# Kernel optimization log

Measured on AMD Instinct MI355X. Metric: run time of the kernel, lower is better.

The kernel has to match this reference:

```python
import jax, jax.numpy as jnp
import numpy as np

B, DIM, H, W = 8, 96, 256, 256
NH, WS, SS = 3, 8, 4
HD = DIM // NH
SCALE = HD ** -0.5
N = WS * WS  # tokens per window


def _rel_pos_log(ws):
    # [N, N, 2] signed log relative coordinates (matches get_relative_positions)
    coords = np.stack(np.meshgrid(np.arange(ws), np.arange(ws), indexing='ij'))
    cf = coords.reshape(2, -1)
    rel = (cf[:, :, None] - cf[:, None, :]).transpose(1, 2, 0).astype(np.float32)
    return np.sign(rel) * np.log1p(np.abs(rel))


def _attn_mask(Hh, Ww, ws, ss):
    # Swin shifted-window mask: [nW, N, N] with 0 / -100
    img = np.zeros((Hh, Ww))
    cnt = 0
    sl = (slice(0, -ws), slice(-ws, -ss), slice(-ss, None))
    for h in sl:
        for w in sl:
            img[h, w] = cnt
            cnt += 1
    mw = img.reshape(Hh // ws, ws, Ww // ws, ws).transpose(0, 2, 1, 3).reshape(-1, ws * ws)
    am = mw[:, None, :] - mw[:, :, None]
    return np.where(am != 0, -100.0, 0.0).astype(np.float32)


REL_POS = jnp.asarray(_rel_pos_log(WS))        # [N, N, 2]
ATTN_MASK = jnp.asarray(_attn_mask(H, W, WS, SS))  # [nW, N, N]


def setup_inputs() -> dict:
    key = jax.random.key(0)
    ks = jax.random.split(key, 8)
    s = 0.02
    return {
        'x': jax.random.normal(ks[0], (B, DIM, H, W), jnp.float32),
        'V_w': jax.random.normal(ks[1], (DIM, DIM), jnp.float32) * s,
        'V_b': jnp.zeros((DIM,), jnp.float32),
        'QK_w': jax.random.normal(ks[2], (2 * DIM, DIM), jnp.float32) * s,
        'QK_b': jnp.zeros((2 * DIM,), jnp.float32),
        'proj_w': jax.random.normal(ks[3], (DIM, DIM), jnp.float32) * s,
        'proj_b': jnp.zeros((DIM,), jnp.float32),
        'dw_w': jax.random.normal(ks[4], (DIM, 5, 5), jnp.float32) * s,
        'dw_b': jnp.zeros((DIM,), jnp.float32),
        'meta_w1': jax.random.normal(ks[5], (256, 2), jnp.float32) * 0.1,
        'meta_b1': jnp.zeros((256,), jnp.float32),
        'meta_w2': jax.random.normal(ks[6], (NH, 256), jnp.float32) * 0.1,
        'meta_b2': jnp.zeros((NH,), jnp.float32),
    }


def reference(x, V_w, V_b, QK_w, QK_b, proj_w, proj_b, dw_w, dw_b,
              meta_w1, meta_b1, meta_w2, meta_b2):
    # 1x1 convs as channel matmuls
    V = jnp.einsum('bchw,oc->bohw', x, V_w) + V_b[None, :, None, None]
    QK = jnp.einsum('bchw,oc->bohw', x, QK_w) + QK_b[None, :, None, None]
    qkv = jnp.concatenate([QK, V], axis=1).transpose(0, 2, 3, 1)  # [B,H,W,3C]
    # cyclic shift
    qkv = jnp.roll(qkv, (-SS, -SS), axis=(1, 2))
    # window partition -> [B*nW, N, 3C]
    xw = qkv.reshape(B, H // WS, WS, W // WS, WS, 3 * DIM)
    xw = xw.transpose(0, 1, 3, 2, 4, 5).reshape(-1, N, 3 * DIM)
    qkv3 = xw.reshape(-1, N, 3, NH, HD).transpose(2, 0, 3, 1, 4)  # [3, B_, nh, N, hd]
    q, k, v = qkv3[0] * SCALE, qkv3[1], qkv3[2]
    attn = jnp.einsum('whnd,whmd->whnm', q, k)  # [B_, nh, N, N]
    # MLP relative-position bias
    bias = jax.nn.relu(REL_POS @ meta_w1.T + meta_b1) @ meta_w2.T + meta_b2  # [N,N,nh]
    attn = attn + bias.transpose(2, 0, 1)[None]
    nW = ATTN_MASK.shape[0]
    attn = attn.reshape(B, nW, NH, N, N) + ATTN_MASK[None, :, None]
    attn = jax.nn.softmax(attn, axis=-1).reshape(-1, NH, N, N)
    xo = jnp.einsum('whnm,whmd->wnhd', attn, v).reshape(-1, N, DIM)
    # window reverse -> [B,H,W,C]
    xr = xo.reshape(B, H // WS, W // WS, WS, WS, DIM)
    xr = xr.transpose(0, 1, 3, 2, 4, 5).reshape(B, H, W, DIM)
    xr = jnp.roll(xr, (SS, SS), axis=(1, 2)).transpose(0, 3, 1, 2)  # [B,C,H,W]
    # depthwise 5x5 conv with reflect padding on V
    Vp = jnp.pad(V, ((0, 0), (0, 0), (2, 2), (2, 2)), mode='reflect')
    conv_out = jax.lax.conv_general_dilated(
        Vp, dw_w.reshape(DIM, 1, 5, 5), (1, 1), 'VALID',
        feature_group_count=DIM,
        dimension_numbers=('NCHW', 'OIHW', 'NCHW')) + dw_b[None, :, None, None]
    out = jnp.einsum('bchw,oc->bohw', conv_out + xr, proj_w) + proj_b[None, :, None, None]
    return out
```

## Files before the change

### kernel.cpp

```cpp
#include <hip/hip_runtime.h>
#include <hip/hip_bf16.h>

#define HW 65536
#define SCALE_Q 0.17677669529663687f

typedef __bf16 bf16x8 __attribute__((ext_vector_type(8)));
typedef float f32x4 __attribute__((ext_vector_type(4)));

__global__ void bias_kernel(const float* __restrict__ w1, const float* __restrict__ b1,
                            const float* __restrict__ w2, const float* __restrict__ b2,
                            float* __restrict__ biasF) {
    int gid = blockIdx.x * blockDim.x + threadIdx.x;
    if (gid >= 12288) return;
    int lane = gid & 63, r = (gid >> 6) & 3, ni = (gid >> 8) & 3, mi = (gid >> 10) & 3, h = gid >> 12;
    int i = mi * 16 + ((lane >> 4) << 2) + r;
    int j = ni * 16 + (lane & 15);
    float di = (float)((i >> 3) - (j >> 3));
    float dj = (float)((i & 7) - (j & 7));
    float r0 = (di > 0.f ? 1.f : (di < 0.f ? -1.f : 0.f)) * log1pf(fabsf(di));
    float r1 = (dj > 0.f ? 1.f : (dj < 0.f ? -1.f : 0.f)) * log1pf(fabsf(dj));
    float acc = 0.f;
    for (int t = 0; t < 256; ++t) {
        float u = fmaf(w1[2 * t], r0, fmaf(w1[2 * t + 1], r1, b1[t]));
        u = fmaxf(u, 0.f);
        acc = fmaf(w2[h * 256 + t], u, acc);
    }
    biasF[gid] = acc + b2[h];
}

__global__ void wtrans_kernel(const float* __restrict__ QK_w, const float* __restrict__ V_w,
                              const float* __restrict__ proj_w,
                              __bf16* __restrict__ Whi, __bf16* __restrict__ Wlo,
                              __bf16* __restrict__ WpHi, __bf16* __restrict__ WpLo) {
    int idx = blockIdx.x * blockDim.x + threadIdx.x;
    if (idx < 288 * 96) {
        int oo = idx / 96, c = idx - oo * 96;
        int h = oo / 96, rem = oo - h * 96, grp = rem >> 5, d = rem & 31;
        float w = (grp == 0) ? QK_w[(h * 32 + d) * 96 + c]
                : (grp == 1) ? QK_w[(96 + h * 32 + d) * 96 + c]
                             : V_w[(h * 32 + d) * 96 + c];
        __bf16 hi = (__bf16)w;
        Whi[idx] = hi;
        Wlo[idx] = (__bf16)(w - (float)hi);
    } else if (idx < 288 * 96 + 96 * 96) {
        int rdx = idx - 288 * 96;
        float w = proj_w[rdx];
        __bf16 hi = (__bf16)w;
        WpHi[rdx] = hi;
        WpLo[rdx] = (__bf16)(w - (float)hi);
    }
}

template <bool XRB>
__global__ __launch_bounds__(256, 4) void fused_qkv_attn(
    const float* __restrict__ x,
    const __bf16* __restrict__ Whi, const __bf16* __restrict__ Wlo,
    const float* __restrict__ QK_b, const float* __restrict__ V_b,
    const float* __restrict__ biasF,
    unsigned short* __restrict__ Vout, void* __restrict__ xrv) {
    __shared__ __align__(16) char lds[39936];
    int tid = threadIdx.x;
    int w4 = tid >> 6;
    int lane = tid & 63;
    int l16 = lane & 15;
    int g8 = (lane >> 4) << 3;
    int g4 = (lane >> 4) << 2;
    int bx0 = blockIdx.x;
    int bxs = (bx0 & 7) * 256 + (bx0 >> 3);
    int b = bxs >> 8;
    int wh = (bxs >> 3) & 31;
    int ww0 = (bxs & 7) << 2;
    int wh8 = wh << 3;
    int ww = ww0 + w4;
    int ti = lane >> 3, tj = lane & 7;
    int ph = (wh8 + ti + 4) & 255;
    int pw = ((ww << 3) + tj + 4) & 255;
    int pos   = ph * 256 + pw;
    int pos_s = (wh8 + ti) * 256 + (ww << 3) + tj;

    const float* xb = x + (size_t)b * 96 * HW;
    bf16x8 Ah[4][3];
#pragma unroll
    for (int mi = 0; mi < 4; ++mi) {
        int t = mi * 16 + l16;
        int py = (wh8 + (t >> 3) + 4) & 255;
        int px = ((ww << 3) + (t & 7) + 4) & 255;
        const float* xp = xb + py * 256 + px + (size_t)g8 * HW;
#pragma unroll
        for (int ks = 0; ks < 3; ++ks)
#pragma unroll
            for (int e = 0; e < 8; ++e)
                Ah[mi][ks][e] = (__bf16)xp[(size_t)(ks * 32 + e) * HW];
    }

    char* hb = lds + w4 * 9984;
    __bf16* slab = (__bf16*)hb;
    __bf16* Vt   = (__bf16*)(hb + 5120);
    float*  Xr   = (float*)hb;

    bool bhh = (wh == 31), bww = (ww == 31);
    int rc[4];
#pragma unroll
    for (int ni = 0; ni < 4; ++ni) {
        int t = ni * 16 + l16;
        rc[ni] = (bhh ? (((t >> 3) < 4) ? 1 : 2) : 0) * 3 + (bww ? (((t & 7) < 4) ? 1 : 2) : 0);
    }

#pragma unroll 1
    for (int h = 0; h < 3; ++h) {
        bf16x8 Qf[4], Kf[4];
        {
            f32x4 acc[4][2];
#pragma unroll
            for (int mi = 0; mi < 4; ++mi)
#pragma unroll
                for (int ni = 0; ni < 2; ++ni) acc[mi][ni] = (f32x4){0.f, 0.f, 0.f, 0.f};
            __builtin_amdgcn_s_setprio(1);
#pragma unroll
            for (int ks = 0; ks < 3; ++ks)
#pragma unroll
                for (int ni = 0; ni < 2; ++ni) {
                    bf16x8 Bh = *(const bf16x8*)(Whi + (h * 96 + ni * 16 + l16) * 96 + ks * 32 + g8);
#pragma unroll
                    for (int mi = 0; mi < 4; ++mi)
                        acc[mi][ni] = __builtin_amdgcn_mfma_f32_16x16x32_bf16(Ah[mi][ks], Bh, acc[mi][ni], 0, 0, 0);
                }
            __builtin_amdgcn_s_setprio(0);
#pragma unroll
            for (int ni = 0; ni < 2; ++ni) {
                float bias = QK_b[h * 32 + ni * 16 + l16];
#pragma unroll
                for (int mi = 0; mi < 4; ++mi)
#pragma unroll
                    for (int r = 0; r < 4; ++r)
                        slab[(mi * 16 + g4 + r) * 40 + ni * 16 + l16] = (__bf16)((acc[mi][ni][r] + bias) * SCALE_Q);
            }
#pragma unroll
            for (int mi = 0; mi < 4; ++mi) Qf[mi] = *(const bf16x8*)(slab + (mi * 16 + l16) * 40 + g8);
        }
        {
            f32x4 acc[4][2];
#pragma unroll
            for (int mi = 0; mi < 4; ++mi)
#pragma unroll
                for (int ni = 0; ni < 2; ++ni) acc[mi][ni] = (f32x4){0.f, 0.f, 0.f, 0.f};
            __builtin_amdgcn_s_setprio(1);
#pragma unroll
            for (int ks = 0; ks < 3; ++ks)
#pragma unroll
                for (int ni = 0; ni < 2; ++ni) {
                    bf16x8 Bh = *(const bf16x8*)(Whi + (h * 96 + 32 + ni * 16 + l16) * 96 + ks * 32 + g8);
#pragma unroll
                    for (int mi = 0; mi < 4; ++mi)
                        acc[mi][ni] = __builtin_amdgcn_mfma_f32_16x16x32_bf16(Ah[mi][ks], Bh, acc[mi][ni], 0, 0, 0);
                }
            __builtin_amdgcn_s_setprio(0);
#pragma unroll
            for (int ni = 0; ni < 2; ++ni) {
                float bias = QK_b[96 + h * 32 + ni * 16 + l16];
#pragma unroll
                for (int mi = 0; mi < 4; ++mi)
#pragma unroll
                    for (int r = 0; r < 4; ++r)
                        slab[(mi * 16 + g4 + r) * 40 + ni * 16 + l16] = (__bf16)(acc[mi][ni][r] + bias);
            }
#pragma unroll
            for (int mi = 0; mi < 4; ++mi) Kf[mi] = *(const bf16x8*)(slab + (mi * 16 + l16) * 40 + g8);
        }
        {
            f32x4 acc[4][2];
#pragma unroll
            for (int mi = 0; mi < 4; ++mi)
#pragma unroll
                for (int ni = 0; ni < 2; ++ni) acc[mi][ni] = (f32x4){0.f, 0.f, 0.f, 0.f};
            __builtin_amdgcn_s_setprio(1);
#pragma unroll
            for (int ks = 0; ks < 3; ++ks)
#pragma unroll
                for (int ni = 0; ni < 2; ++ni) {
                    bf16x8 Bh = *(const bf16x8*)(Whi + (h * 96 + 64 + ni * 16 + l16) * 96 + ks * 32 + g8);
#pragma unroll
                    for (int mi = 0; mi < 4; ++mi)
                        acc[mi][ni] = __builtin_amdgcn_mfma_f32_16x16x32_bf16(Ah[mi][ks], Bh, acc[mi][ni], 0, 0, 0);
                }
            __builtin_amdgcn_s_setprio(0);
#pragma unroll
            for (int ni = 0; ni < 2; ++ni) {
                float bias = V_b[h * 32 + ni * 16 + l16];
#pragma unroll
                for (int mi = 0; mi < 4; ++mi)
#pragma unroll
                    for (int r = 0; r < 4; ++r)
                        Vt[(ni * 16 + l16) * 72 + mi * 16 + g4 + r] = (__bf16)(acc[mi][ni][r] + bias);
            }
        }
#pragma unroll
        for (int d = 0; d < 32; ++d)
            Vout[(size_t)(b * 96 + h * 32 + d) * HW + pos_s] = ((const unsigned short*)Vt)[d * 72 + lane];

        f32x4 sc[4][4];
        __builtin_amdgcn_s_setprio(1);
#pragma unroll
        for (int mi = 0; mi < 4; ++mi)
#pragma unroll
            for (int ni = 0; ni < 4; ++ni) {
                sc[mi][ni] = (f32x4){0.f, 0.f, 0.f, 0.f};
                sc[mi][ni] = __builtin_amdgcn_mfma_f32_16x16x32_bf16(Qf[mi], Kf[ni], sc[mi][ni], 0, 0, 0);
            }
        __builtin_amdgcn_s_setprio(0);
        const float* bF = biasF + h * 4096;
#pragma unroll
        for (int mi = 0; mi < 4; ++mi)
#pragma unroll
            for (int r = 0; r < 4; ++r) {
                int row = mi * 16 + g4 + r;
                float s0 = sc[mi][0][r] + bF[((mi * 4 + 0) * 4 + r) * 64 + lane];
                float s1 = sc[mi][1][r] + bF[((mi * 4 + 1) * 4 + r) * 64 + lane];
                float s2 = sc[mi][2][r] + bF[((mi * 4 + 2) * 4 + r) * 64 + lane];
                float s3 = sc[mi][3][r] + bF[((mi * 4 + 3) * 4 + r) * 64 + lane];
                if (bhh || bww) {
                    int rr = (bhh ? (((row >> 3) < 4) ? 1 : 2) : 0) * 3 +
                             (bww ? (((row & 7) < 4) ? 1 : 2) : 0);
                    if (rr != rc[0]) s0 -= 100.f;
                    if (rr != rc[1]) s1 -= 100.f;
                    if (rr != rc[2]) s2 -= 100.f;
                    if (rr != rc[3]) s3 -= 100.f;
                }
                float mm = fmaxf(fmaxf(s0, s1), fmaxf(s2, s3));
                mm = fmaxf(mm, __shfl_xor(mm, 1));
                mm = fmaxf(mm, __shfl_xor(mm, 2));
                mm = fmaxf(mm, __shfl_xor(mm, 4));
                mm = fmaxf(mm, __shfl_xor(mm, 8));
                float e0 = __expf(s0 - mm), e1 = __expf(s1 - mm);
                float e2 = __expf(s2 - mm), e3 = __expf(s3 - mm);
                float sum = e0 + e1 + e2 + e3;
                sum += __shfl_xor(sum, 1);
                sum += __shfl_xor(sum, 2);
                sum += __shfl_xor(sum, 4);
                sum += __shfl_xor(sum, 8);
                float inv = 1.f / sum;
                sc[mi][0][r] = e0 * inv;
                sc[mi][1][r] = e1 * inv;
                sc[mi][2][r] = e2 * inv;
                sc[mi][3][r] = e3 * inv;
            }
        f32x4 po[4][2];
#pragma unroll
        for (int mi = 0; mi < 4; ++mi)
#pragma unroll
            for (int ni = 0; ni < 2; ++ni) po[mi][ni] = (f32x4){0.f, 0.f, 0.f, 0.f};
#pragma unroll
        for (int ks = 0; ks < 2; ++ks) {
#pragma unroll
            for (int mi = 0; mi < 4; ++mi)
#pragma unroll
                for (int r = 0; r < 4; ++r) {
                    int row = mi * 16 + g4 + r;
                    slab[row * 40 + l16]      = (__bf16)sc[mi][ks * 2 + 0][r];
                    slab[row * 40 + 16 + l16] = (__bf16)sc[mi][ks * 2 + 1][r];
                }
            bf16x8 Vf[2], Pf;
#pragma unroll
            for (int ni = 0; ni < 2; ++ni)
                Vf[ni] = *(const bf16x8*)(Vt + (ni * 16 + l16) * 72 + ks * 32 + g8);
            __builtin_amdgcn_s_setprio(1);
#pragma unroll
            for (int mi = 0; mi < 4; ++mi) {
                Pf = *(const bf16x8*)(slab + (mi * 16 + l16) * 40 + g8);
#pragma unroll
                for (int ni = 0; ni < 2; ++ni)
                    po[mi][ni] = __builtin_amdgcn_mfma_f32_16x16x32_bf16(Pf, Vf[ni], po[mi][ni], 0, 0, 0);
            }
            __builtin_amdgcn_s_setprio(0);
        }
#pragma unroll
        for (int mi = 0; mi < 4; ++mi)
#pragma unroll
            for (int ni = 0; ni < 2; ++ni)
#pragma unroll
                for (int r = 0; r < 4; ++r)
                    Xr[(mi * 16 + g4 + r) * 36 + ni * 16 + l16] = po[mi][ni][r];
        if constexpr (XRB) {
            unsigned short* xrg = (unsigned short*)xrv + (size_t)(b * 96 + h * 32) * HW + pos;
#pragma unroll
            for (int c4 = 0; c4 < 8; ++c4) {
                f32x4 v = *(const f32x4*)(Xr + lane * 36 + c4 * 4);
#pragma unroll
                for (int j = 0; j < 4; ++j) {
                    __bf16 t = (__bf16)v[j];
                    xrg[(size_t)(c4 * 4 + j) * HW] = *(unsigned short*)&t;
                }
            }
        } else {
            float* xrg = (float*)xrv + (size_t)(b * 96 + h * 32) * HW + pos;
#pragma unroll
            for (int c4 = 0; c4 < 8; ++c4) {
                f32x4 v = *(const f32x4*)(Xr + lane * 36 + c4 * 4);
                xrg[(size_t)(c4 * 4 + 0) * HW] = v[0];
                xrg[(size_t)(c4 * 4 + 1) * HW] = v[1];
                xrg[(size_t)(c4 * 4 + 2) * HW] = v[2];
                xrg[(size_t)(c4 * 4 + 3) * HW] = v[3];
            }
        }
    }
}

template <bool XRB>
__global__ __launch_bounds__(256) void dwproj_kernel(
    const __hip_bfloat16* __restrict__ Vs, const float* __restrict__ dw_w,
    const float* __restrict__ dw_b, const __bf16* __restrict__ WpHi,
    const __bf16* __restrict__ WpLo, const float* __restrict__ pb,
    const void* __restrict__ xrv, float* __restrict__ T) {
    __shared__ __align__(16) __bf16 Ts[13312];
    int bx0 = blockIdx.x;
    int bx = (bx0 & 7) * 512 + (bx0 >> 3);
    int half = bx & 1, h = (bx >> 1) & 255, b = bx >> 9;
    int w0 = half << 7;
    int tid = threadIdx.x;
    for (int task = tid; task < 1536; task += 256) {
        int c = task >> 4, g = task & 15;
        int wbase = w0 + (g << 3);
        const __hip_bfloat16* Vp = Vs + (size_t)(b * 96 + c) * HW;
        const float* wt = dw_w + c * 25;
        float acc[8];
        float bias = dw_b[c];
#pragma unroll
        for (int i = 0; i < 8; ++i) acc[i] = bias;
        bool fast = (wbase >= 8) && (wbase <= 240);
#pragma unroll
        for (int dy = -2; dy <= 2; ++dy) {
            int hh = h + dy;
            hh = hh < 0 ? -hh : (hh > 255 ? 510 - hh : hh);
            int hs = (hh + 252) & 255;
            const __hip_bfloat16* row = Vp + hs * 256;
            float xv[12];
            if (fast) {
                const uint* rp = (const uint*)(row + (wbase - 6));
#pragma unroll
                for (int g2 = 0; g2 < 6; ++g2) {
                    uint u = rp[g2];
                    xv[2 * g2]     = __uint_as_float(u << 16);
                    xv[2 * g2 + 1] = __uint_as_float(u & 0xffff0000u);
                }
            } else {
#pragma unroll
                for (int idx = 0; idx < 12; ++idx) {
                    int cw = wbase - 2 + idx;
                    cw = cw < 0 ? -cw : (cw > 255 ? 510 - cw : cw);
                    int cs = (cw + 252) & 255;
                    uint u = *(const unsigned short*)(row + cs);
                    xv[idx] = __uint_as_float(u << 16);
                }
            }
            const float* w5 = wt + (dy + 2) * 5;
#pragma unroll
            for (int dx = 0; dx < 5; ++dx) {
                float wv = w5[dx];
#pragma unroll
                for (int i = 0; i < 8; ++i) acc[i] = fmaf(wv, xv[i + dx], acc[i]);
            }
        }
        if constexpr (XRB) {
            const unsigned short* xp = (const unsigned short*)xrv + (size_t)(b * 96 + c) * HW + h * 256 + wbase;
            uint4 u = *(const uint4*)xp;
            acc[0] += __uint_as_float(u.x << 16);
            acc[1] += __uint_as_float(u.x & 0xffff0000u);
            acc[2] += __uint_as_float(u.y << 16);
            acc[3] += __uint_as_float(u.y & 0xffff0000u);
            acc[4] += __uint_as_float(u.z << 16);
            acc[5] += __uint_as_float(u.z & 0xffff0000u);
            acc[6] += __uint_as_float(u.w << 16);
            acc[7] += __uint_as_float(u.w & 0xffff0000u);
        } else {
            const float* xp = (const float*)xrv + (size_t)(b * 96 + c) * HW + h * 256;
            f32x4 x0 = *(const f32x4*)(xp + wbase);
            f32x4 x1 = *(const f32x4*)(xp + wbase + 4);
#pragma unroll
            for (int i = 0; i < 4; ++i) { acc[i] += x0[i]; acc[4 + i] += x1[i]; }
        }
#pragma unroll
        for (int i = 0; i < 8; ++i) Ts[(g * 8 + i) * 104 + c] = (__bf16)acc[i];
    }
    __syncthreads();
    int lane = tid & 63;
    int l16 = lane & 15;
    int g8 = (lane >> 4) << 3;
    int g4 = (lane >> 4) << 2;
    int wv = tid >> 6;
    f32x4 po[2][6];
#pragma unroll
    for (int mi = 0; mi < 2; ++mi)
#pragma unroll
        for (int ni = 0; ni < 6; ++ni) po[mi][ni] = (f32x4){0.f, 0.f, 0.f, 0.f};
#pragma unroll
    for (int ks = 0; ks < 3; ++ks) {
        bf16x8 Av[2];
#pragma unroll
        for (int mi = 0; mi < 2; ++mi)
            Av[mi] = *(const bf16x8*)(Ts + (wv * 32 + mi * 16 + l16) * 104 + ks * 32 + g8);
#pragma unroll
        for (int ni = 0; ni < 6; ++ni) {
            int o = ni * 16 + l16;
            bf16x8 Bh = *(const bf16x8*)(WpHi + o * 96 + ks * 32 + g8);
            bf16x8 Bl = *(const bf16x8*)(WpLo + o * 96 + ks * 32 + g8);
#pragma unroll
            for (int mi = 0; mi < 2; ++mi) {
                po[mi][ni] = __builtin_amdgcn_mfma_f32_16x16x32_bf16(Av[mi], Bh, po[mi][ni], 0, 0, 0);
                po[mi][ni] = __builtin_amdgcn_mfma_f32_16x16x32_bf16(Av[mi], Bl, po[mi][ni], 0, 0, 0);
            }
        }
    }
#pragma unroll
    for (int ni = 0; ni < 6; ++ni) {
        int o = ni * 16 + l16;
        float bias = pb[o];
#pragma unroll
        for (int mi = 0; mi < 2; ++mi) {
            f32x4 v = po[mi][ni];
            v[0] += bias; v[1] += bias; v[2] += bias; v[3] += bias;
            *(f32x4*)(T + (size_t)(b * 96 + o) * HW + h * 256 + w0 + wv * 32 + mi * 16 + g4) = v;
        }
    }
}

extern "C" void kernel_launch(void* const* d_in, const int* in_sizes, int n_in,
                              void* d_out, int out_size, void* d_ws, size_t ws_size,
                              hipStream_t stream) {
    const float* x      = (const float*)d_in[0];
    const float* V_w    = (const float*)d_in[1];
    const float* V_b    = (const float*)d_in[2];
    const float* QK_w   = (const float*)d_in[3];
    const float* QK_b   = (const float*)d_in[4];
    const float* proj_w = (const float*)d_in[5];
    const float* proj_b = (const float*)d_in[6];
    const float* dw_w   = (const float*)d_in[7];
    const float* dw_b   = (const float*)d_in[8];
    const float* mw1    = (const float*)d_in[9];
    const float* mb1    = (const float*)d_in[10];
    const float* mw2    = (const float*)d_in[11];
    const float* mb2    = (const float*)d_in[12];
    float* out = (float*)d_out;

    char* ws = (char*)d_ws;
    const size_t VB = 100663296;
    bool xrb = (ws_size >= 2 * VB + 49152 + 2 * 55296 + 2 * 18432);

    __hip_bfloat16* Vbuf = (__hip_bfloat16*)ws;
    size_t off = VB;
    unsigned short* xr16 = nullptr;
    if (xrb) { xr16 = (unsigned short*)(ws + off); off += VB; }
    float*  biasF = (float*)(ws + off); off += 49152;
    __bf16* Whi   = (__bf16*)(ws + off); off += 55296;
    __bf16* Wlo   = (__bf16*)(ws + off); off += 55296;
    __bf16* WpHi  = (__bf16*)(ws + off); off += 18432;
    __bf16* WpLo  = (__bf16*)(ws + off);

    bias_kernel<<<48, 256, 0, stream>>>(mw1, mb1, mw2, mb2, biasF);
    wtrans_kernel<<<144, 256, 0, stream>>>(QK_w, V_w, proj_w, Whi, Wlo, WpHi, WpLo);
    if (xrb) {
        fused_qkv_attn<true><<<2048, 256, 0, stream>>>(x, Whi, Wlo, QK_b, V_b, biasF,
                                                       (unsigned short*)Vbuf, (void*)xr16);
        dwproj_kernel<true><<<4096, 256, 0, stream>>>(Vbuf, dw_w, dw_b, WpHi, WpLo, proj_b,
                                                      (const void*)xr16, out);
    } else {
        fused_qkv_attn<false><<<2048, 256, 0, stream>>>(x, Whi, Wlo, QK_b, V_b, biasF,
                                                        (unsigned short*)Vbuf, (void*)out);
        dwproj_kernel<false><<<4096, 256, 0, stream>>>(Vbuf, dw_w, dw_b, WpHi, WpLo, proj_b,
                                                       (const void*)out, out);
    }
}
```

Baseline: 676.0 us.

## Pre-transpose x into window-major bf16 layout and store attention output window-major

Adds an xprep kernel that gathers the shifted-window tiles of x into a contiguous bf16 window-major buffer, so the fused attention kernel loads its A fragments with vector loads instead of strided scalar fp32 gathers. The attention output is also written in a window-major bf16 layout through LDS, and the depthwise/projection kernel reads that layout back. The projection kernel moves to 512 threads with one 16-row tile per wave. This costs an extra kernel launch, an extra full pass over x, and a third 100MB workspace buffer, and the new path only runs when the workspace is large enough.

Result: slower. 729.1 us (+7.8%).

```diff
diff --git a/kernel.cpp b/kernel.cpp
--- a/kernel.cpp
+++ b/kernel.cpp
@@ -51,9 +51,37 @@
     }
 }
 
-template <bool XRB>
+__global__ __launch_bounds__(256) void xprep_kernel(const float* __restrict__ x,
+                                                    __bf16* __restrict__ xT) {
+    __shared__ __bf16 Xs[26624];
+    int tid = threadIdx.x;
+    int bxs = blockIdx.x;
+    int b = bxs >> 8;
+    int wh = (bxs >> 3) & 31;
+    int ww0 = (bxs & 7) << 2;
+    int wh8 = wh << 3, wb8 = ww0 << 3;
+    const float* xb = x + (size_t)b * 96 * HW;
+    for (int idx = tid; idx < 24576; idx += 256) {
+        int c = idx >> 8, r = (idx >> 5) & 7, col = idx & 31;
+        int pph = (wh8 + r + 4) & 255;
+        int ppw = (wb8 + col + 4) & 255;
+        Xs[(col >> 3) * 6656 + (r * 8 + (col & 7)) * 104 + c] =
+            (__bf16)xb[(size_t)c * HW + pph * 256 + ppw];
+    }
+    __syncthreads();
+    int win = tid >> 6, t = tid & 63;
+    const __bf16* row = Xs + win * 6656 + t * 104;
+    __bf16* dst = xT + (size_t)(b * 1024 + wh * 32 + ww0 + win) * 6144 + t * 8;
+#pragma unroll
+    for (int ks = 0; ks < 3; ++ks)
+#pragma unroll
+        for (int g = 0; g < 4; ++g)
+            *(bf16x8*)(dst + (ks * 4 + g) * 512) = *(const bf16x8*)(row + ks * 32 + g * 8);
+}
+
+template <int MODE>
 __global__ __launch_bounds__(256, 4) void fused_qkv_attn(
-    const float* __restrict__ x,
+    const float* __restrict__ x, const __bf16* __restrict__ xT,
     const __bf16* __restrict__ Whi, const __bf16* __restrict__ Wlo,
     const float* __restrict__ QK_b, const float* __restrict__ V_b,
     const float* __restrict__ biasF,
@@ -72,25 +100,35 @@
     int ww0 = (bxs & 7) << 2;
     int wh8 = wh << 3;
     int ww = ww0 + w4;
+    int wl = wh * 32 + ww;
     int ti = lane >> 3, tj = lane & 7;
     int ph = (wh8 + ti + 4) & 255;
     int pw = ((ww << 3) + tj + 4) & 255;
     int pos   = ph * 256 + pw;
     int pos_s = (wh8 + ti) * 256 + (ww << 3) + tj;
 
-    const float* xb = x + (size_t)b * 96 * HW;
     bf16x8 Ah[4][3];
-#pragma unroll
-    for (int mi = 0; mi < 4; ++mi) {
-        int t = mi * 16 + l16;
-        int py = (wh8 + (t >> 3) + 4) & 255;
-        int px = ((ww << 3) + (t & 7) + 4) & 255;
-        const float* xp = xb + py * 256 + px + (size_t)g8 * HW;
-#pragma unroll
-        for (int ks = 0; ks < 3; ++ks)
-#pragma unroll
-            for (int e = 0; e < 8; ++e)
-                Ah[mi][ks][e] = (__bf16)xp[(size_t)(ks * 32 + e) * HW];
+    if constexpr (MODE == 2) {
+        const __bf16* xTw = xT + (size_t)(b * 1024 + wl) * 6144;
+#pragma unroll
+        for (int mi = 0; mi < 4; ++mi)
+#pragma unroll
+            for (int ks = 0; ks < 3; ++ks)
+                Ah[mi][ks] = *(const bf16x8*)(xTw + (ks * 4 + (lane >> 4)) * 512 + (mi * 16 + l16) * 8);
+    } else {
+        const float* xb = x + (size_t)b * 96 * HW;
+#pragma unroll
+        for (int mi = 0; mi < 4; ++mi) {
+            int t = mi * 16 + l16;
+            int py = (wh8 + (t >> 3) + 4) & 255;
+            int px = ((ww << 3) + (t & 7) + 4) & 255;
+            const float* xp = xb + py * 256 + px + (size_t)g8 * HW;
+#pragma unroll
+            for (int ks = 0; ks < 3; ++ks)
+#pragma unroll
+                for (int e = 0; e < 8; ++e)
+                    Ah[mi][ks][e] = (__bf16)xp[(size_t)(ks * 32 + e) * HW];
+        }
     }
 
     char* hb = lds + w4 * 9984;
@@ -273,40 +311,58 @@
             }
             __builtin_amdgcn_s_setprio(0);
         }
-#pragma unroll
-        for (int mi = 0; mi < 4; ++mi)
-#pragma unroll
-            for (int ni = 0; ni < 2; ++ni)
-#pragma unroll
-                for (int r = 0; r < 4; ++r)
-                    Xr[(mi * 16 + g4 + r) * 36 + ni * 16 + l16] = po[mi][ni][r];
-        if constexpr (XRB) {
-            unsigned short* xrg = (unsigned short*)xrv + (size_t)(b * 96 + h * 32) * HW + pos;
-#pragma unroll
-            for (int c4 = 0; c4 < 8; ++c4) {
-                f32x4 v = *(const f32x4*)(Xr + lane * 36 + c4 * 4);
-#pragma unroll
-                for (int j = 0; j < 4; ++j) {
-                    __bf16 t = (__bf16)v[j];
-                    xrg[(size_t)(c4 * 4 + j) * HW] = *(unsigned short*)&t;
-                }
-            }
+        if constexpr (MODE == 2) {
+            __bf16* Xrt = slab;
+#pragma unroll
+            for (int mi = 0; mi < 4; ++mi)
+#pragma unroll
+                for (int ni = 0; ni < 2; ++ni)
+#pragma unroll
+                    for (int r = 0; r < 4; ++r)
+                        Xrt[(ni * 16 + l16) * 72 + mi * 16 + g4 + r] = (__bf16)po[mi][ni][r];
+            int d = lane >> 1, half = lane & 1;
+            const unsigned short* src = (const unsigned short*)Xrt + d * 72 + half * 32;
+            unsigned short* dst = (unsigned short*)xrv +
+                ((size_t)(b * 96 + h * 32 + d) * 1024 + wl) * 64 + half * 32;
+#pragma unroll
+            for (int i = 0; i < 4; ++i)
+                *(uint4*)(dst + i * 8) = *(const uint4*)(src + i * 8);
         } else {
-            float* xrg = (float*)xrv + (size_t)(b * 96 + h * 32) * HW + pos;
-#pragma unroll
-            for (int c4 = 0; c4 < 8; ++c4) {
-                f32x4 v = *(const f32x4*)(Xr + lane * 36 + c4 * 4);
-                xrg[(size_t)(c4 * 4 + 0) * HW] = v[0];
-                xrg[(size_t)(c4 * 4 + 1) * HW] = v[1];
-                xrg[(size_t)(c4 * 4 + 2) * HW] = v[2];
-                xrg[(size_t)(c4 * 4 + 3) * HW] = v[3];
+#pragma unroll
+            for (int mi = 0; mi < 4; ++mi)
+#pragma unroll
+                for (int ni = 0; ni < 2; ++ni)
+#pragma unroll
+                    for (int r = 0; r < 4; ++r)
+                        Xr[(mi * 16 + g4 + r) * 36 + ni * 16 + l16] = po[mi][ni][r];
+            if constexpr (MODE == 1) {
+                unsigned short* xrg = (unsigned short*)xrv + (size_t)(b * 96 + h * 32) * HW + pos;
+#pragma unroll
+                for (int c4 = 0; c4 < 8; ++c4) {
+                    f32x4 v = *(const f32x4*)(Xr + lane * 36 + c4 * 4);
+#pragma unroll
+                    for (int j = 0; j < 4; ++j) {
+                        __bf16 t = (__bf16)v[j];
+                        xrg[(size_t)(c4 * 4 + j) * HW] = *(unsigned short*)&t;
+                    }
+                }
+            } else {
+                float* xrg = (float*)xrv + (size_t)(b * 96 + h * 32) * HW + pos;
+#pragma unroll
+                for (int c4 = 0; c4 < 8; ++c4) {
+                    f32x4 v = *(const f32x4*)(Xr + lane * 36 + c4 * 4);
+                    xrg[(size_t)(c4 * 4 + 0) * HW] = v[0];
+                    xrg[(size_t)(c4 * 4 + 1) * HW] = v[1];
+                    xrg[(size_t)(c4 * 4 + 2) * HW] = v[2];
+                    xrg[(size_t)(c4 * 4 + 3) * HW] = v[3];
+                }
             }
         }
     }
 }
 
-template <bool XRB>
-__global__ __launch_bounds__(256) void dwproj_kernel(
+template <int MODE>
+__global__ __launch_bounds__(512) void dwproj_kernel(
     const __hip_bfloat16* __restrict__ Vs, const float* __restrict__ dw_w,
     const float* __restrict__ dw_b, const __bf16* __restrict__ WpHi,
     const __bf16* __restrict__ WpLo, const float* __restrict__ pb,
@@ -317,7 +373,7 @@
     int half = bx & 1, h = (bx >> 1) & 255, b = bx >> 9;
     int w0 = half << 7;
     int tid = threadIdx.x;
-    for (int task = tid; task < 1536; task += 256) {
+    for (int task = tid; task < 1536; task += 512) {
         int c = task >> 4, g = task & 15;
         int wbase = w0 + (g << 3);
         const __hip_bfloat16* Vp = Vs + (size_t)(b * 96 + c) * HW;
@@ -360,7 +416,23 @@
                 for (int i = 0; i < 8; ++i) acc[i] = fmaf(wv, xv[i + dx], acc[i]);
             }
         }
-        if constexpr (XRB) {
+        if constexpr (MODE == 2) {
+            int hs2 = (h + 252) & 255;
+            int ps2 = (wbase + 252) & 255;
+            int wrow = (hs2 >> 3) * 32;
+            int rowoff = (hs2 & 7) * 8;
+            const unsigned short* base = (const unsigned short*)xrv + (size_t)(b * 96 + c) * HW;
+            uint2 A = *(const uint2*)(base + (size_t)(wrow + (ps2 >> 3)) * 64 + rowoff + 4);
+            uint2 B = *(const uint2*)(base + (size_t)(wrow + (wbase >> 3)) * 64 + rowoff);
+            acc[0] += __uint_as_float(A.x << 16);
+            acc[1] += __uint_as_float(A.x & 0xffff0000u);
+            acc[2] += __uint_as_float(A.y << 16);
+            acc[3] += __uint_as_float(A.y & 0xffff0000u);
+            acc[4] += __uint_as_float(B.x << 16);
+            acc[5] += __uint_as_float(B.x & 0xffff0000u);
+            acc[6] += __uint_as_float(B.y << 16);
+            acc[7] += __uint_as_float(B.y & 0xffff0000u);
+        } else if constexpr (MODE == 1) {
             const unsigned short* xp = (const unsigned short*)xrv + (size_t)(b * 96 + c) * HW + h * 256 + wbase;
             uint4 u = *(const uint4*)xp;
             acc[0] += __uint_as_float(u.x << 16);
@@ -387,39 +459,28 @@
     int g8 = (lane >> 4) << 3;
     int g4 = (lane >> 4) << 2;
     int wv = tid >> 6;
-    f32x4 po[2][6];
-#pragma unroll
-    for (int mi = 0; mi < 2; ++mi)
-#pragma unroll
-        for (int ni = 0; ni < 6; ++ni) po[mi][ni] = (f32x4){0.f, 0.f, 0.f, 0.f};
+    f32x4 po[6];
+#pragma unroll
+    for (int ni = 0; ni < 6; ++ni) po[ni] = (f32x4){0.f, 0.f, 0.f, 0.f};
 #pragma unroll
     for (int ks = 0; ks < 3; ++ks) {
-        bf16x8 Av[2];
-#pragma unroll
-        for (int mi = 0; mi < 2; ++mi)
-            Av[mi] = *(const bf16x8*)(Ts + (wv * 32 + mi * 16 + l16) * 104 + ks * 32 + g8);
+        bf16x8 Av = *(const bf16x8*)(Ts + (wv * 16 + l16) * 104 + ks * 32 + g8);
 #pragma unroll
         for (int ni = 0; ni < 6; ++ni) {
             int o = ni * 16 + l16;
             bf16x8 Bh = *(const bf16x8*)(WpHi + o * 96 + ks * 32 + g8);
             bf16x8 Bl = *(const bf16x8*)(WpLo + o * 96 + ks * 32 + g8);
-#pragma unroll
-            for (int mi = 0; mi < 2; ++mi) {
-                po[mi][ni] = __builtin_amdgcn_mfma_f32_16x16x32_bf16(Av[mi], Bh, po[mi][ni], 0, 0, 0);
-                po[mi][ni] = __builtin_amdgcn_mfma_f32_16x16x32_bf16(Av[mi], Bl, po[mi][ni], 0, 0, 0);
-            }
+            po[ni] = __builtin_amdgcn_mfma_f32_16x16x32_bf16(Av, Bh, po[ni], 0, 0, 0);
+            po[ni] = __builtin_amdgcn_mfma_f32_16x16x32_bf16(Av, Bl, po[ni], 0, 0, 0);
         }
     }
 #pragma unroll
     for (int ni = 0; ni < 6; ++ni) {
         int o = ni * 16 + l16;
         float bias = pb[o];
-#pragma unroll
-        for (int mi = 0; mi < 2; ++mi) {
-            f32x4 v = po[mi][ni];
-            v[0] += bias; v[1] += bias; v[2] += bias; v[3] += bias;
-            *(f32x4*)(T + (size_t)(b * 96 + o) * HW + h * 256 + w0 + wv * 32 + mi * 16 + g4) = v;
-        }
+        f32x4 v = po[ni];
+        v[0] += bias; v[1] += bias; v[2] += bias; v[3] += bias;
+        *(f32x4*)(T + (size_t)(b * 96 + o) * HW + h * 256 + w0 + wv * 16 + g4) = v;
     }
 }
 
@@ -443,12 +504,15 @@
 
     char* ws = (char*)d_ws;
     const size_t VB = 100663296;
-    bool xrb = (ws_size >= 2 * VB + 49152 + 2 * 55296 + 2 * 18432);
+    const size_t TAB = 49152 + 2 * 55296 + 2 * 18432;
+    int mode = (ws_size >= 3 * VB + TAB) ? 2 : (ws_size >= 2 * VB + TAB) ? 1 : 0;
 
     __hip_bfloat16* Vbuf = (__hip_bfloat16*)ws;
     size_t off = VB;
     unsigned short* xr16 = nullptr;
-    if (xrb) { xr16 = (unsigned short*)(ws + off); off += VB; }
+    __bf16* xT = nullptr;
+    if (mode >= 1) { xr16 = (unsigned short*)(ws + off); off += VB; }
+    if (mode == 2) { xT = (__bf16*)(ws + off); off += VB; }
     float*  biasF = (float*)(ws + off); off += 49152;
     __bf16* Whi   = (__bf16*)(ws + off); off += 55296;
     __bf16* Wlo   = (__bf16*)(ws + off); off += 55296;
@@ -457,15 +521,21 @@
 
     bias_kernel<<<48, 256, 0, stream>>>(mw1, mb1, mw2, mb2, biasF);
     wtrans_kernel<<<144, 256, 0, stream>>>(QK_w, V_w, proj_w, Whi, Wlo, WpHi, WpLo);
-    if (xrb) {
-        fused_qkv_attn<true><<<2048, 256, 0, stream>>>(x, Whi, Wlo, QK_b, V_b, biasF,
-                                                       (unsigned short*)Vbuf, (void*)xr16);
-        dwproj_kernel<true><<<4096, 256, 0, stream>>>(Vbuf, dw_w, dw_b, WpHi, WpLo, proj_b,
-                                                      (const void*)xr16, out);
+    if (mode == 2) {
+        xprep_kernel<<<2048, 256, 0, stream>>>(x, xT);
+        fused_qkv_attn<2><<<2048, 256, 0, stream>>>(x, xT, Whi, Wlo, QK_b, V_b, biasF,
+                                                    (unsigned short*)Vbuf, (void*)xr16);
+        dwproj_kernel<2><<<4096, 512, 0, stream>>>(Vbuf, dw_w, dw_b, WpHi, WpLo, proj_b,
+                                                   (const void*)xr16, out);
+    } else if (mode == 1) {
+        fused_qkv_attn<1><<<2048, 256, 0, stream>>>(x, nullptr, Whi, Wlo, QK_b, V_b, biasF,
+                                                    (unsigned short*)Vbuf, (void*)xr16);
+        dwproj_kernel<1><<<4096, 512, 0, stream>>>(Vbuf, dw_w, dw_b, WpHi, WpLo, proj_b,
+                                                   (const void*)xr16, out);
     } else {
-        fused_qkv_attn<false><<<2048, 256, 0, stream>>>(x, Whi, Wlo, QK_b, V_b, biasF,
-                                                        (unsigned short*)Vbuf, (void*)out);
-        dwproj_kernel<false><<<4096, 256, 0, stream>>>(Vbuf, dw_w, dw_b, WpHi, WpLo, proj_b,
-                                                       (const void*)out, out);
+        fused_qkv_attn<0><<<2048, 256, 0, stream>>>(x, nullptr, Whi, Wlo, QK_b, V_b, biasF,
+                                                    (unsigned short*)Vbuf, (void*)out);
+        dwproj_kernel<0><<<4096, 512, 0, stream>>>(Vbuf, dw_w, dw_b, WpHi, WpLo, proj_b,
+                                                   (const void*)out, out);
     }
 }
```

## Store attention output in window-major bf16 layout and swizzle dwproj LDS tile

Applied to the files above, without the earlier changes.

The attention kernel now transposes its bf16 window output through LDS and writes each channel's 64-token window as contiguous 16-byte vector stores in a window-major layout. The old path was scattered 2-byte stores strided by HW per channel. The dwproj kernel reads this layout back, splitting each 8-pixel chunk across two shifted windows. Its LDS staging tile also gets an XOR swizzle to cut bank conflicts on the strided writes and MFMA operand reads. The cost is more complex address arithmetic and narrower 8-byte gathered loads in dwproj.

New measurement: 646.6 us (median of 2 runs). 4.4% less time.

```diff
diff --git a/kernel.cpp b/kernel.cpp
--- a/kernel.cpp
+++ b/kernel.cpp
@@ -51,7 +51,7 @@
     }
 }
 
-template <bool XRB>
+template <int MODE>
 __global__ __launch_bounds__(256, 4) void fused_qkv_attn(
     const float* __restrict__ x,
     const __bf16* __restrict__ Whi, const __bf16* __restrict__ Wlo,
@@ -72,6 +72,7 @@
     int ww0 = (bxs & 7) << 2;
     int wh8 = wh << 3;
     int ww = ww0 + w4;
+    int wl = wh * 32 + ww;
     int ti = lane >> 3, tj = lane & 7;
     int ph = (wh8 + ti + 4) & 255;
     int pw = ((ww << 3) + tj + 4) & 255;
@@ -273,25 +274,30 @@
             }
             __builtin_amdgcn_s_setprio(0);
         }
-#pragma unroll
-        for (int mi = 0; mi < 4; ++mi)
-#pragma unroll
-            for (int ni = 0; ni < 2; ++ni)
-#pragma unroll
-                for (int r = 0; r < 4; ++r)
-                    Xr[(mi * 16 + g4 + r) * 36 + ni * 16 + l16] = po[mi][ni][r];
-        if constexpr (XRB) {
-            unsigned short* xrg = (unsigned short*)xrv + (size_t)(b * 96 + h * 32) * HW + pos;
-#pragma unroll
-            for (int c4 = 0; c4 < 8; ++c4) {
-                f32x4 v = *(const f32x4*)(Xr + lane * 36 + c4 * 4);
-#pragma unroll
-                for (int j = 0; j < 4; ++j) {
-                    __bf16 t = (__bf16)v[j];
-                    xrg[(size_t)(c4 * 4 + j) * HW] = *(unsigned short*)&t;
-                }
-            }
+        if constexpr (MODE == 1) {
+            __bf16* Xrt = slab;
+#pragma unroll
+            for (int mi = 0; mi < 4; ++mi)
+#pragma unroll
+                for (int ni = 0; ni < 2; ++ni)
+#pragma unroll
+                    for (int r = 0; r < 4; ++r)
+                        Xrt[(ni * 16 + l16) * 72 + mi * 16 + g4 + r] = (__bf16)po[mi][ni][r];
+            int d = lane >> 1, half = lane & 1;
+            const unsigned short* src = (const unsigned short*)Xrt + d * 72 + half * 32;
+            unsigned short* dst = (unsigned short*)xrv +
+                ((size_t)(b * 96 + h * 32 + d) * 1024 + wl) * 64 + half * 32;
+#pragma unroll
+            for (int i = 0; i < 4; ++i)
+                *(uint4*)(dst + i * 8) = *(const uint4*)(src + i * 8);
         } else {
+#pragma unroll
+            for (int mi = 0; mi < 4; ++mi)
+#pragma unroll
+                for (int ni = 0; ni < 2; ++ni)
+#pragma unroll
+                    for (int r = 0; r < 4; ++r)
+                        Xr[(mi * 16 + g4 + r) * 36 + ni * 16 + l16] = po[mi][ni][r];
             float* xrg = (float*)xrv + (size_t)(b * 96 + h * 32) * HW + pos;
 #pragma unroll
             for (int c4 = 0; c4 < 8; ++c4) {
@@ -305,13 +311,14 @@
     }
 }
 
-template <bool XRB>
+template <int MODE>
 __global__ __launch_bounds__(256) void dwproj_kernel(
     const __hip_bfloat16* __restrict__ Vs, const float* __restrict__ dw_w,
     const float* __restrict__ dw_b, const __bf16* __restrict__ WpHi,
     const __bf16* __restrict__ WpLo, const float* __restrict__ pb,
     const void* __restrict__ xrv, float* __restrict__ T) {
     __shared__ __align__(16) __bf16 Ts[13312];
+    char* Tsb = (char*)Ts;
     int bx0 = blockIdx.x;
     int bx = (bx0 & 7) * 512 + (bx0 >> 3);
     int half = bx & 1, h = (bx >> 1) & 255, b = bx >> 9;
@@ -360,17 +367,22 @@
                 for (int i = 0; i < 8; ++i) acc[i] = fmaf(wv, xv[i + dx], acc[i]);
             }
         }
-        if constexpr (XRB) {
-            const unsigned short* xp = (const unsigned short*)xrv + (size_t)(b * 96 + c) * HW + h * 256 + wbase;
-            uint4 u = *(const uint4*)xp;
-            acc[0] += __uint_as_float(u.x << 16);
-            acc[1] += __uint_as_float(u.x & 0xffff0000u);
-            acc[2] += __uint_as_float(u.y << 16);
-            acc[3] += __uint_as_float(u.y & 0xffff0000u);
-            acc[4] += __uint_as_float(u.z << 16);
-            acc[5] += __uint_as_float(u.z & 0xffff0000u);
-            acc[6] += __uint_as_float(u.w << 16);
-            acc[7] += __uint_as_float(u.w & 0xffff0000u);
+        if constexpr (MODE == 1) {
+            int hs2 = (h + 252) & 255;
+            int ps2 = (wbase + 252) & 255;
+            int wrow = (hs2 >> 3) * 32;
+            int rowoff = (hs2 & 7) * 8;
+            const unsigned short* base = (const unsigned short*)xrv + (size_t)(b * 96 + c) * HW;
+            uint2 A = *(const uint2*)(base + (size_t)(wrow + (ps2 >> 3)) * 64 + rowoff + 4);
+            uint2 B = *(const uint2*)(base + (size_t)(wrow + (wbase >> 3)) * 64 + rowoff);
+            acc[0] += __uint_as_float(A.x << 16);
+            acc[1] += __uint_as_float(A.x & 0xffff0000u);
+            acc[2] += __uint_as_float(A.y << 16);
+            acc[3] += __uint_as_float(A.y & 0xffff0000u);
+            acc[4] += __uint_as_float(B.x << 16);
+            acc[5] += __uint_as_float(B.x & 0xffff0000u);
+            acc[6] += __uint_as_float(B.y << 16);
+            acc[7] += __uint_as_float(B.y & 0xffff0000u);
         } else {
             const float* xp = (const float*)xrv + (size_t)(b * 96 + c) * HW + h * 256;
             f32x4 x0 = *(const f32x4*)(xp + wbase);
@@ -379,7 +391,10 @@
             for (int i = 0; i < 4; ++i) { acc[i] += x0[i]; acc[4 + i] += x1[i]; }
         }
 #pragma unroll
-        for (int i = 0; i < 8; ++i) Ts[(g * 8 + i) * 104 + c] = (__bf16)acc[i];
+        for (int i = 0; i < 8; ++i) {
+            int px = g * 8 + i;
+            *(__bf16*)(Tsb + (((px * 104 + c) * 2) ^ ((g & 7) << 4))) = (__bf16)acc[i];
+        }
     }
     __syncthreads();
     int lane = tid & 63;
@@ -396,8 +411,10 @@
     for (int ks = 0; ks < 3; ++ks) {
         bf16x8 Av[2];
 #pragma unroll
-        for (int mi = 0; mi < 2; ++mi)
-            Av[mi] = *(const bf16x8*)(Ts + (wv * 32 + mi * 16 + l16) * 104 + ks * 32 + g8);
+        for (int mi = 0; mi < 2; ++mi) {
+            int px = wv * 32 + mi * 16 + l16;
+            Av[mi] = *(const bf16x8*)(Tsb + (((px * 104 + ks * 32 + g8) * 2) ^ (((px >> 3) & 7) << 4)));
+        }
 #pragma unroll
         for (int ni = 0; ni < 6; ++ni) {
             int o = ni * 16 + l16;
@@ -443,12 +460,13 @@
 
     char* ws = (char*)d_ws;
     const size_t VB = 100663296;
-    bool xrb = (ws_size >= 2 * VB + 49152 + 2 * 55296 + 2 * 18432);
+    const size_t TAB = 49152 + 2 * 55296 + 2 * 18432;
+    int mode = (ws_size >= 2 * VB + TAB) ? 1 : 0;
 
     __hip_bfloat16* Vbuf = (__hip_bfloat16*)ws;
     size_t off = VB;
     unsigned short* xr16 = nullptr;
-    if (xrb) { xr16 = (unsigned short*)(ws + off); off += VB; }
+    if (mode == 1) { xr16 = (unsigned short*)(ws + off); off += VB; }
     float*  biasF = (float*)(ws + off); off += 49152;
     __bf16* Whi   = (__bf16*)(ws + off); off += 55296;
     __bf16* Wlo   = (__bf16*)(ws + off); off += 55296;
@@ -457,15 +475,15 @@
 
     bias_kernel<<<48, 256, 0, stream>>>(mw1, mb1, mw2, mb2, biasF);
     wtrans_kernel<<<144, 256, 0, stream>>>(QK_w, V_w, proj_w, Whi, Wlo, WpHi, WpLo);
-    if (xrb) {
-        fused_qkv_attn<true><<<2048, 256, 0, stream>>>(x, Whi, Wlo, QK_b, V_b, biasF,
-                                                       (unsigned short*)Vbuf, (void*)xr16);
-        dwproj_kernel<true><<<4096, 256, 0, stream>>>(Vbuf, dw_w, dw_b, WpHi, WpLo, proj_b,
-                                                      (const void*)xr16, out);
+    if (mode == 1) {
+        fused_qkv_attn<1><<<2048, 256, 0, stream>>>(x, Whi, Wlo, QK_b, V_b, biasF,
+                                                    (unsigned short*)Vbuf, (void*)xr16);
+        dwproj_kernel<1><<<4096, 256, 0, stream>>>(Vbuf, dw_w, dw_b, WpHi, WpLo, proj_b,
+                                                   (const void*)xr16, out);
     } else {
-        fused_qkv_attn<false><<<2048, 256, 0, stream>>>(x, Whi, Wlo, QK_b, V_b, biasF,
-                                                        (unsigned short*)Vbuf, (void*)out);
-        dwproj_kernel<false><<<4096, 256, 0, stream>>>(Vbuf, dw_w, dw_b, WpHi, WpLo, proj_b,
-                                                       (const void*)out, out);
+        fused_qkv_attn<0><<<2048, 256, 0, stream>>>(x, Whi, Wlo, QK_b, V_b, biasF,
+                                                    (unsigned short*)Vbuf, (void*)out);
+        dwproj_kernel<0><<<4096, 256, 0, stream>>>(Vbuf, dw_w, dw_b, WpHi, WpLo, proj_b,
+                                                   (const void*)out, out);
     }
 }
```
